# Optimization experiments

Hardware: AMD Instinct MI355X
Metric: run time of the kernel (lower is better)

The kernel has to match this reference:

```python
import jax, jax.numpy as jnp
import numpy as np

B, T, H, S, NH = 8, 4096, 1024, 64, 16
DH = H // NH
L = T // S  # tokens per sentence (contiguous partition)


def setup_inputs() -> dict:
    key = jax.random.key(0)
    ks = jax.random.split(key, 10)
    init = lambda k, shape: (jax.random.normal(k, shape, dtype=jnp.float32) * 0.02)
    starts = jnp.arange(S, dtype=jnp.int32) * L
    bounds = jnp.stack([starts, starts + L], axis=-1)  # [S,2]
    sentence_boundaries = jnp.broadcast_to(bounds, (B, S, 2))
    return {
        "context_hidden": jax.random.normal(ks[0], (B, T, H), dtype=jnp.float32),
        "sentence_boundaries": sentence_boundaries,
        "in_proj_w": init(ks[1], (3 * H, H)),
        "in_proj_b": jnp.zeros((3 * H,), jnp.float32),
        "out_w": init(ks[2], (H, H)),
        "out_b": jnp.zeros((H,), jnp.float32),
        "w1": init(ks[3], (H, 2 * H)),
        "b1": jnp.zeros((H,), jnp.float32),
        "w2": init(ks[4], (1, H)),
        "b2": jnp.zeros((1,), jnp.float32),
    }


def _forward(h, sentence_boundaries, in_proj_w, in_proj_b, out_w, out_b, w1, b1, w2, b2):
    starts = sentence_boundaries[:, :, 0]  # [B,S]
    ends = sentence_boundaries[:, :, 1]    # [B,S]
    t = jnp.arange(T, dtype=jnp.int32)
    # membership: token t belongs to sentence s iff start <= t < end
    member = (t[None, :, None] >= starts[:, None, :]) & (t[None, :, None] < ends[:, None, :])  # [B,T,S]
    mf = member.astype(h.dtype)
    counts = jnp.clip(mf.sum(axis=1), 1.0)  # [B,S]
    # segment mean pooling (encode_sentences)
    sent_repr = jnp.einsum('bts,bth->bsh', mf, h) / counts[..., None]  # [B,S,H]

    # multihead self-attention over sentence reprs (eval mode, no dropout)
    qkv = sent_repr @ in_proj_w.T + in_proj_b  # [B,S,3H]
    q, k, v = jnp.split(qkv, 3, axis=-1)
    q = q.reshape(B, S, NH, DH)
    k = k.reshape(B, S, NH, DH)
    v = v.reshape(B, S, NH, DH)
    scores = jnp.einsum('bqhd,bkhd->bhqk', q, k) / jnp.sqrt(jnp.asarray(DH, h.dtype))
    attn = jax.nn.softmax(scores, axis=-1)
    ctx = jnp.einsum('bhqk,bkhd->bqhd', attn, v).reshape(B, S, H)
    attended = ctx @ out_w.T + out_b  # [B,S,H]

    # gather each token's sentence repr
    sid = jnp.clip(member.astype(jnp.int32).argmax(axis=-1), 0, S - 1)  # [B,T]
    covered = member.any(axis=-1)  # [B,T]
    att_tok = jnp.take_along_axis(attended, sid[..., None], axis=1)  # [B,T,H]

    # coherence scorer MLP on concat([token, sent_repr]) without materializing concat
    hid = jax.nn.relu(h @ w1[:, :H].T + att_tok @ w1[:, H:].T + b1)  # [B,T,H]
    score = (hid @ w2.T + b2)[..., 0]  # [B,T]
    score = jnp.where(covered, score, 0.0)
    return h + score[..., None] * h


def reference(context_hidden, sentence_boundaries, in_proj_w, in_proj_b, out_w, out_b, w1, b1, w2, b2):
    return _forward(context_hidden, sentence_boundaries, in_proj_w, in_proj_b,
                    out_w, out_b, w1, b1, w2, b2)
```

## Files before the change

kernel.cpp:

```cpp
#include <hip/hip_runtime.h>
#include <stdint.h>

#define BB 8
#define TT 4096
#define HH 1024
#define SS 64
#define NHH 16
#define DHH 64

typedef __attribute__((ext_vector_type(8))) short short8;
typedef __attribute__((ext_vector_type(8))) unsigned short ushortx8;
typedef __attribute__((ext_vector_type(4))) float f32x4;
typedef unsigned short u16;

#define GLOAD16(gp, lp)                                                   \
  __builtin_amdgcn_global_load_lds(                                      \
      (const __attribute__((address_space(1))) void*)(gp),               \
      (__attribute__((address_space(3))) void*)(lp), 16, 0, 0)

__device__ __forceinline__ u16 f2bf(float f) {
  union { float f; uint32_t u; } v;
  v.f = f;
  uint32_t u = v.u;
  uint32_t r = u + 0x7fffu + ((u >> 16) & 1u);
  return (u16)(r >> 16);
}

__device__ __forceinline__ float bf2f(u16 b) {
  union { uint32_t u; float f; } v;
  v.u = ((uint32_t)b) << 16;
  return v.f;
}

__device__ __forceinline__ void stage_tile(u16* lds, const float* src, int ld, int tid) {
#pragma unroll
  for (int q = 0; q < 4; ++q) {
    int slot_id = tid + (q << 8);
    int row = slot_id >> 3;
    int sl = slot_id & 7;
    const float* p = src + (size_t)row * ld + (sl << 3);
    float4 x0 = *(const float4*)(p);
    float4 x1 = *(const float4*)(p + 4);
    ushortx8 o;
    o[0] = f2bf(x0.x); o[1] = f2bf(x0.y); o[2] = f2bf(x0.z); o[3] = f2bf(x0.w);
    o[4] = f2bf(x1.x); o[5] = f2bf(x1.y); o[6] = f2bf(x1.z); o[7] = f2bf(x1.w);
    *(ushortx8*)(&lds[(row << 6) + (((sl ^ (row & 7)) << 3))]) = o;
  }
}

__global__ __launch_bounds__(256) void conv_tile_kernel(const float* __restrict__ src,
                                                        int ld, int ntile_k,
                                                        u16* __restrict__ dst) {
  int bid = blockIdx.x;
  int rt = bid / ntile_k;
  int kt = bid - rt * ntile_k;
  const float* s0 = src + (size_t)rt * 128 * ld + kt * 64;
  u16* d0 = dst + (size_t)bid * 8192;
  int tid = threadIdx.x;
#pragma unroll
  for (int q = 0; q < 4; ++q) {
    int slot_id = tid + (q << 8);
    int row = slot_id >> 3;
    int sl = slot_id & 7;
    const float* p = s0 + (size_t)row * ld + (sl << 3);
    float4 x0 = *(const float4*)(p);
    float4 x1 = *(const float4*)(p + 4);
    ushortx8 o;
    o[0] = f2bf(x0.x); o[1] = f2bf(x0.y); o[2] = f2bf(x0.z); o[3] = f2bf(x0.w);
    o[4] = f2bf(x1.x); o[5] = f2bf(x1.y); o[6] = f2bf(x1.z); o[7] = f2bf(x1.w);
    *(ushortx8*)(&d0[(row << 6) + (((sl ^ (row & 7)) << 3))]) = o;
  }
}

__global__ __launch_bounds__(256) void pool_bf_kernel(const u16* __restrict__ hbf,
                                                      const int* __restrict__ bounds,
                                                      float* __restrict__ sent) {
  int bs = blockIdx.x;
  int b = bs >> 6;
  int start = bounds[bs * 2];
  int end = bounds[bs * 2 + 1];
  int lo = max(start, 0), hi = min(end, TT);
  int cnt = max(hi - lo, 0);
  float inv = 1.0f / (float)max(cnt, 1);
  int tid = threadIdx.x;
  int sg = tid >> 1;
  int half = tid & 1;
  int kt = sg >> 3, slot = sg & 7;
  float a[8] = {};
  for (int t = lo + half; t < hi; t += 2) {
    int grow = b * TT + t;
    int rt = grow >> 7, r = grow & 127;
    const u16* tile = hbf + ((size_t)rt * 16 + kt) * 8192;
    ushortx8 v = *(const ushortx8*)(&tile[(r << 6) + ((slot ^ (r & 7)) << 3)]);
#pragma unroll
    for (int j = 0; j < 8; ++j) a[j] += bf2f(v[j]);
  }
#pragma unroll
  for (int j = 0; j < 8; ++j) a[j] += __shfl_xor(a[j], 1);
  if (half == 0) {
    float* d = sent + (size_t)bs * HH + sg * 8;
#pragma unroll
    for (int j = 0; j < 8; ++j) d[j] = a[j] * inv;
  }
}

__global__ __launch_bounds__(256) void setup_misc(const float* __restrict__ ipb,
                                                  const float* __restrict__ outb,
                                                  const float* __restrict__ b1,
                                                  const int* __restrict__ bounds,
                                                  float* __restrict__ qkv,
                                                  float* __restrict__ att,
                                                  float* __restrict__ cbuf,
                                                  int* __restrict__ sid) {
  int idx = blockIdx.x * 256 + threadIdx.x;
  const int STR = 2048 * 256;
  for (int i = idx; i < 512 * 3072; i += STR) qkv[i] = ipb[i % 3072];
  for (int i = idx; i < 512 * 1024; i += STR) att[i] = outb[i & 1023];
  for (int i = idx; i < 512 * 1024; i += STR) cbuf[i] = b1[i & 1023];
  if (idx < BB * TT) {
    int b = idx >> 12, t = idx & (TT - 1);
    int r = -1;
    for (int s = 0; s < SS; ++s) {
      int st = bounds[(b * SS + s) * 2], en = bounds[(b * SS + s) * 2 + 1];
      if (t >= st && t < en) { r = s; break; }
    }
    sid[idx] = r;
  }
}

__global__ __launch_bounds__(256) void gemm_bt_atomic(const float* __restrict__ A, int lda,
                                                      const float* __restrict__ Bm, int ldb,
                                                      float* __restrict__ C, int ldc,
                                                      int kper) {
  __shared__ u16 As[128 * 64];
  __shared__ u16 Bs[128 * 64];
  int tid = threadIdx.x;
  int m0 = blockIdx.x * 128, n0 = blockIdx.y * 128;
  int kbeg = blockIdx.z * kper;
  f32x4 acc[4][4] = {};

  for (int k0 = kbeg; k0 < kbeg + kper; k0 += 64) {
    __syncthreads();
    stage_tile(As, A + (size_t)m0 * lda + k0, lda, tid);
    stage_tile(Bs, Bm + (size_t)n0 * ldb + k0, ldb, tid);
    __syncthreads();
    int lane = tid & 63, wid = tid >> 6;
    int wm = wid >> 1, wn = wid & 1;
    int lr = lane & 15, lg = lane >> 4;
#pragma unroll
    for (int kk = 0; kk < 2; ++kk) {
      short8 af[4], bfr[4];
#pragma unroll
      for (int i = 0; i < 4; ++i) {
        int arow = wm * 64 + i * 16 + lr;
        int aslot = (kk * 4 + lg) ^ (arow & 7);
        af[i] = *(const short8*)(&As[(arow << 6) + (aslot << 3)]);
        int brow = wn * 64 + i * 16 + lr;
        int bslot = (kk * 4 + lg) ^ (brow & 7);
        bfr[i] = *(const short8*)(&Bs[(brow << 6) + (bslot << 3)]);
      }
#pragma unroll
      for (int i = 0; i < 4; ++i)
#pragma unroll
        for (int j = 0; j < 4; ++j)
          acc[i][j] = __builtin_amdgcn_mfma_f32_16x16x32_bf16(af[i], bfr[j], acc[i][j], 0, 0, 0);
    }
  }

  int lane = tid & 63, wid = tid >> 6;
  int wm = wid >> 1, wn = wid & 1;
  int lr = lane & 15, lg = lane >> 4;
#pragma unroll
  for (int i = 0; i < 4; ++i)
#pragma unroll
    for (int j = 0; j < 4; ++j)
#pragma unroll
      for (int r = 0; r < 4; ++r) {
        int row = m0 + wm * 64 + i * 16 + lg * 4 + r;
        int col = n0 + wn * 64 + j * 16 + lr;
        atomicAdd(&C[(size_t)row * ldc + col], acc[i][j][r]);
      }
}

__global__ __launch_bounds__(256) void attn_kernel(const float* __restrict__ qkv,
                                                   float* __restrict__ ctx) {
  int bh = blockIdx.x;
  int b = bh >> 4, nh = bh & 15;
  __shared__ float q[64][64], k[64][64], v[64][64], s[64][64];
  int tid = threadIdx.x;
  const float* base = qkv + (size_t)b * SS * 3072 + nh * 64;
  for (int e = tid; e < 4096; e += 256) {
    int i = e >> 6, d = e & 63;
    q[i][d] = base[(size_t)i * 3072 + d];
    k[i][d] = base[(size_t)i * 3072 + 1024 + d];
    v[i][d] = base[(size_t)i * 3072 + 2048 + d];
  }
  __syncthreads();
  for (int e = tid; e < 4096; e += 256) {
    int i = e >> 6, j = e & 63;
    float acc = 0.f;
#pragma unroll 8
    for (int d = 0; d < 64; ++d) acc += q[i][d] * k[j][d];
    s[i][j] = acc * 0.125f;
  }
  __syncthreads();
  {
    int r = tid >> 2, sub = tid & 3;
    int j0 = sub * 16;
    float m = -1e30f;
#pragma unroll
    for (int j = 0; j < 16; ++j) m = fmaxf(m, s[r][j0 + j]);
    m = fmaxf(m, __shfl_xor(m, 1));
    m = fmaxf(m, __shfl_xor(m, 2));
    float sum = 0.f;
#pragma unroll
    for (int j = 0; j < 16; ++j) {
      float e_ = __expf(s[r][j0 + j] - m);
      s[r][j0 + j] = e_;
      sum += e_;
    }
    sum += __shfl_xor(sum, 1);
    sum += __shfl_xor(sum, 2);
    float inv = 1.0f / sum;
#pragma unroll
    for (int j = 0; j < 16; ++j) s[r][j0 + j] *= inv;
  }
  __syncthreads();
  for (int e = tid; e < 4096; e += 256) {
    int i = e >> 6, d = e & 63;
    float acc = 0.f;
#pragma unroll 8
    for (int j = 0; j < 64; ++j) acc += s[i][j] * v[j][d];
    ctx[((size_t)b * SS + i) * HH + nh * 64 + d] = acc;
  }
}

__global__ __launch_bounds__(512, 6) void score_partial(const u16* __restrict__ hbf,
                                                        const u16* __restrict__ wbf,
                                                        const float* __restrict__ cbuf,
                                                        const float* __restrict__ w2,
                                                        const int* __restrict__ sid_arr,
                                                        float* __restrict__ score_part) {
  __shared__ u16 As[8192];
  __shared__ u16 Bs[8192];
  __shared__ float w2_lds[128];
  __shared__ int sid_lds[128];
  __shared__ float red[128];

  int tid = threadIdx.x;
  int bid = blockIdx.x;
  int x = bid & 7;
  int g = bid >> 3;
  int mt = x * 32 + (g >> 3);
  int c = g & 7;
  int n0 = c * 128;
  size_t g0 = (size_t)mt * 128;
  int b = (int)(g0 >> 12);
  const u16* asrc = hbf + (size_t)mt * 16 * 8192;
  const u16* bsrc = wbf + (size_t)c * 16 * 8192;

  if (tid < 128) {
    w2_lds[tid] = w2[n0 + tid];
    sid_lds[tid] = sid_arr[g0 + tid];
    red[tid] = 0.f;
  }

  int lane = tid & 63, wid = tid >> 6;
  int wm = wid >> 2, wn = wid & 3;
  int lr = lane & 15, lg = lane >> 4;

  f32x4 acc[4][2] = {};
  for (int kt = 0; kt < 16; ++kt) {
    __syncthreads();
    const u16* at = asrc + kt * 8192;
    const u16* bt = bsrc + kt * 8192;
#pragma unroll
    for (int q = 0; q < 2; ++q) {
      int base = q * 4096 + wid * 512;
      GLOAD16(at + base + lane * 8, &As[base]);
      GLOAD16(bt + base + lane * 8, &Bs[base]);
    }
    __syncthreads();
#pragma unroll
    for (int kk = 0; kk < 2; ++kk) {
      short8 af[4], bfr[2];
#pragma unroll
      for (int i = 0; i < 4; ++i) {
        int arow = wm * 64 + i * 16 + lr;
        int aslot = (kk * 4 + lg) ^ (arow & 7);
        af[i] = *(const short8*)(&As[(arow << 6) + (aslot << 3)]);
      }
#pragma unroll
      for (int j = 0; j < 2; ++j) {
        int brow = wn * 32 + j * 16 + lr;
        int bslot = (kk * 4 + lg) ^ (brow & 7);
        bfr[j] = *(const short8*)(&Bs[(brow << 6) + (bslot << 3)]);
      }
#pragma unroll
      for (int i = 0; i < 4; ++i)
#pragma unroll
        for (int j = 0; j < 2; ++j)
          acc[i][j] = __builtin_amdgcn_mfma_f32_16x16x32_bf16(af[i], bfr[j], acc[i][j], 0, 0, 0);
    }
  }

  float sp[4][4];
#pragma unroll
  for (int i = 0; i < 4; ++i) {
#pragma unroll
    for (int r = 0; r < 4; ++r) {
      int rowl = wm * 64 + i * 16 + lg * 4 + r;
      int s = sid_lds[rowl];
      int sc = s < 0 ? 0 : s;
      const float* crow = cbuf + ((size_t)b * SS + sc) * HH + n0;
      float accs = 0.f;
#pragma unroll
      for (int j = 0; j < 2; ++j) {
        int coll = wn * 32 + j * 16 + lr;
        float t = acc[i][j][r] + crow[coll];
        if (t > 0.f) accs += t * w2_lds[coll];
      }
      sp[i][r] = accs;
    }
  }

#pragma unroll
  for (int i = 0; i < 4; ++i)
#pragma unroll
    for (int r = 0; r < 4; ++r) {
      float v = sp[i][r];
      v += __shfl_xor(v, 1);
      v += __shfl_xor(v, 2);
      v += __shfl_xor(v, 4);
      v += __shfl_xor(v, 8);
      sp[i][r] = v;
    }
  if (lr == 0) {
#pragma unroll
    for (int i = 0; i < 4; ++i)
#pragma unroll
      for (int r = 0; r < 4; ++r)
        atomicAdd(&red[wm * 64 + i * 16 + lg * 4 + r], sp[i][r]);
  }
  __syncthreads();
  if (tid < 128) score_part[(size_t)c * (BB * TT) + g0 + tid] = red[tid];
}

__global__ __launch_bounds__(256) void scale_kernel(const float* __restrict__ h,
                                                    const float* __restrict__ score_part,
                                                    const float* __restrict__ b2,
                                                    const int* __restrict__ sid_arr,
                                                    float* __restrict__ out) {
  __shared__ float fac[16];
  int tid = threadIdx.x;
  int r0 = blockIdx.x * 16;
  if (tid < 16) {
    int t = r0 + tid;
    float s = b2[0];
#pragma unroll
    for (int c = 0; c < 8; ++c) s += score_part[(size_t)c * (BB * TT) + t];
    fac[tid] = (sid_arr[t] >= 0) ? (1.0f + s) : 1.0f;
  }
  __syncthreads();
  const float4* h4 = (const float4*)h + (size_t)r0 * 256;
  float4* o4 = (float4*)out + (size_t)r0 * 256;
  for (int e = tid; e < 16 * 256; e += 256) {
    float f = fac[e >> 8];
    float4 v = h4[e];
    v.x *= f; v.y *= f; v.z *= f; v.w *= f;
    o4[e] = v;
  }
}

extern "C" void kernel_launch(void* const* d_in, const int* in_sizes, int n_in,
                              void* d_out, int out_size, void* d_ws, size_t ws_size,
                              hipStream_t stream) {
  const float* h        = (const float*)d_in[0];
  const int*   bounds   = (const int*)d_in[1];
  const float* in_proj_w = (const float*)d_in[2];
  const float* in_proj_b = (const float*)d_in[3];
  const float* out_w    = (const float*)d_in[4];
  const float* out_b    = (const float*)d_in[5];
  const float* w1       = (const float*)d_in[6];
  const float* b1       = (const float*)d_in[7];
  const float* w2       = (const float*)d_in[8];
  const float* b2       = (const float*)d_in[9];
  float* out = (float*)d_out;

  char* ws = (char*)d_ws;
  float* sent  = (float*)(ws);
  float* qkv   = (float*)(ws + (2ull << 20));
  float* ctx   = (float*)(ws + (8ull << 20));
  float* att   = (float*)(ws + (10ull << 20));
  float* cbuf  = (float*)(ws + (12ull << 20));
  int*   sid   = (int*)(ws + (14ull << 20));
  float* spart = (float*)(ws + (15ull << 20));
  u16*   hbf   = (u16*)(ws + (16ull << 20));
  u16*   wbf   = (u16*)(ws + (80ull << 20));

  conv_tile_kernel<<<256 * 16, 256, 0, stream>>>(h, HH, 16, hbf);
  conv_tile_kernel<<<8 * 16, 256, 0, stream>>>(w1, 2 * HH, 16, wbf);

  pool_bf_kernel<<<BB * SS, 256, 0, stream>>>(hbf, bounds, sent);
  setup_misc<<<2048, 256, 0, stream>>>(in_proj_b, out_b, b1, bounds, qkv, att, cbuf, sid);

  gemm_bt_atomic<<<dim3(4, 24, 4), 256, 0, stream>>>(sent, HH, in_proj_w, HH, qkv, 3 * HH, 256);
  attn_kernel<<<BB * NHH, 256, 0, stream>>>(qkv, ctx);
  gemm_bt_atomic<<<dim3(4, 8, 4), 256, 0, stream>>>(ctx, HH, out_w, HH, att, HH, 256);
  gemm_bt_atomic<<<dim3(4, 8, 4), 256, 0, stream>>>(att, HH, w1 + HH, 2 * HH, cbuf, HH, 256);

  score_partial<<<2048, 512, 0, stream>>>(hbf, wbf, cbuf, w2, sid, spart);
  scale_kernel<<<2048, 256, 0, stream>>>(h, spart, b2, sid, out);
}
```

Measured before the change: 300.4 us.

## Double-buffer score GEMM loads and fuse final scaling via last-block counter

The score GEMM now stages K-tiles into two LDS buffers two iterations ahead, using explicit vmcnt waits and barriers so global-to-LDS loads overlap MFMA work. The separate scale kernel is removed. Instead, the last of the eight column blocks for each row tile, found through an atomic counter, sums the partial scores and writes the scaled output. This saves a kernel launch and hides load latency. The cost is doubled LDS, lower occupancy (launch bound 6 down to 4), and a serialized tail in the finishing block.

```diff
diff --git a/kernel.cpp b/kernel.cpp
--- a/kernel.cpp
+++ b/kernel.cpp
@@ -17,6 +17,10 @@
   __builtin_amdgcn_global_load_lds(                                      \
       (const __attribute__((address_space(1))) void*)(gp),               \
       (__attribute__((address_space(3))) void*)(lp), 16, 0, 0)
+
+#define WAITVM(n)                                                         \
+  asm volatile("s_waitcnt vmcnt(" #n ")" ::: "memory");                  \
+  __builtin_amdgcn_sched_barrier(0)
 
 __device__ __forceinline__ u16 f2bf(float f) {
   union { float f; uint32_t u; } v;
@@ -111,12 +115,14 @@
                                                   float* __restrict__ qkv,
                                                   float* __restrict__ att,
                                                   float* __restrict__ cbuf,
-                                                  int* __restrict__ sid) {
+                                                  int* __restrict__ sid,
+                                                  int* __restrict__ cnt) {
   int idx = blockIdx.x * 256 + threadIdx.x;
   const int STR = 2048 * 256;
   for (int i = idx; i < 512 * 3072; i += STR) qkv[i] = ipb[i % 3072];
   for (int i = idx; i < 512 * 1024; i += STR) att[i] = outb[i & 1023];
   for (int i = idx; i < 512 * 1024; i += STR) cbuf[i] = b1[i & 1023];
+  if (idx < 256) cnt[idx] = 0;
   if (idx < BB * TT) {
     int b = idx >> 12, t = idx & (TT - 1);
     int r = -1;
@@ -235,17 +241,22 @@
   }
 }
 
-__global__ __launch_bounds__(512, 6) void score_partial(const u16* __restrict__ hbf,
+__global__ __launch_bounds__(512, 4) void score_partial(const u16* __restrict__ hbf,
                                                         const u16* __restrict__ wbf,
                                                         const float* __restrict__ cbuf,
                                                         const float* __restrict__ w2,
                                                         const int* __restrict__ sid_arr,
-                                                        float* __restrict__ score_part) {
-  __shared__ u16 As[8192];
-  __shared__ u16 Bs[8192];
+                                                        const float* __restrict__ h,
+                                                        const float* __restrict__ b2,
+                                                        float* __restrict__ score_part,
+                                                        int* __restrict__ cnt,
+                                                        float* __restrict__ out) {
+  __shared__ u16 Abuf[2][8192];
+  __shared__ u16 Bbuf[2][8192];
   __shared__ float w2_lds[128];
   __shared__ int sid_lds[128];
   __shared__ float red[128];
+  __shared__ int lastflag;
 
   int tid = threadIdx.x;
   int bid = blockIdx.x;
@@ -264,31 +275,43 @@
     sid_lds[tid] = sid_arr[g0 + tid];
     red[tid] = 0.f;
   }
+  asm volatile("s_waitcnt vmcnt(0)" ::: "memory");
+  __builtin_amdgcn_sched_barrier(0);
 
   int lane = tid & 63, wid = tid >> 6;
   int wm = wid >> 2, wn = wid & 3;
   int lr = lane & 15, lg = lane >> 4;
 
+#define STAGE_KT(kt, bufi)                                                \
+  {                                                                       \
+    const u16* at_ = asrc + (kt) * 8192;                                  \
+    const u16* bt_ = bsrc + (kt) * 8192;                                  \
+    _Pragma("unroll")                                                     \
+    for (int q = 0; q < 2; ++q) {                                         \
+      int base_ = q * 4096 + wid * 512;                                   \
+      GLOAD16(at_ + base_ + lane * 8, &Abuf[bufi][base_]);                \
+      GLOAD16(bt_ + base_ + lane * 8, &Bbuf[bufi][base_]);                \
+    }                                                                     \
+  }
+
+  STAGE_KT(0, 0);
+  STAGE_KT(1, 1);
+
   f32x4 acc[4][2] = {};
-  for (int kt = 0; kt < 16; ++kt) {
-    __syncthreads();
-    const u16* at = asrc + kt * 8192;
-    const u16* bt = bsrc + kt * 8192;
-#pragma unroll
-    for (int q = 0; q < 2; ++q) {
-      int base = q * 4096 + wid * 512;
-      GLOAD16(at + base + lane * 8, &As[base]);
-      GLOAD16(bt + base + lane * 8, &Bs[base]);
-    }
-    __syncthreads();
+  for (int i = 0; i < 16; ++i) {
+    if (i < 15) { WAITVM(4); } else { WAITVM(0); }
+    __builtin_amdgcn_s_barrier();
+    __builtin_amdgcn_sched_barrier(0);
+    const u16* As = Abuf[i & 1];
+    const u16* Bs = Bbuf[i & 1];
 #pragma unroll
     for (int kk = 0; kk < 2; ++kk) {
       short8 af[4], bfr[2];
 #pragma unroll
-      for (int i = 0; i < 4; ++i) {
-        int arow = wm * 64 + i * 16 + lr;
+      for (int ii = 0; ii < 4; ++ii) {
+        int arow = wm * 64 + ii * 16 + lr;
         int aslot = (kk * 4 + lg) ^ (arow & 7);
-        af[i] = *(const short8*)(&As[(arow << 6) + (aslot << 3)]);
+        af[ii] = *(const short8*)(&As[(arow << 6) + (aslot << 3)]);
       }
 #pragma unroll
       for (int j = 0; j < 2; ++j) {
@@ -297,12 +320,16 @@
         bfr[j] = *(const short8*)(&Bs[(brow << 6) + (bslot << 3)]);
       }
 #pragma unroll
-      for (int i = 0; i < 4; ++i)
+      for (int ii = 0; ii < 4; ++ii)
 #pragma unroll
         for (int j = 0; j < 2; ++j)
-          acc[i][j] = __builtin_amdgcn_mfma_f32_16x16x32_bf16(af[i], bfr[j], acc[i][j], 0, 0, 0);
-    }
-  }
+          acc[ii][j] = __builtin_amdgcn_mfma_f32_16x16x32_bf16(af[ii], bfr[j], acc[ii][j], 0, 0, 0);
+    }
+    __builtin_amdgcn_s_barrier();
+    __builtin_amdgcn_sched_barrier(0);
+    if (i < 14) STAGE_KT(i + 2, i & 1);
+  }
+#undef STAGE_KT
 
   float sp[4][4];
 #pragma unroll
@@ -344,31 +371,27 @@
   }
   __syncthreads();
   if (tid < 128) score_part[(size_t)c * (BB * TT) + g0 + tid] = red[tid];
-}
-
-__global__ __launch_bounds__(256) void scale_kernel(const float* __restrict__ h,
-                                                    const float* __restrict__ score_part,
-                                                    const float* __restrict__ b2,
-                                                    const int* __restrict__ sid_arr,
-                                                    float* __restrict__ out) {
-  __shared__ float fac[16];
-  int tid = threadIdx.x;
-  int r0 = blockIdx.x * 16;
-  if (tid < 16) {
-    int t = r0 + tid;
-    float s = b2[0];
-#pragma unroll
-    for (int c = 0; c < 8; ++c) s += score_part[(size_t)c * (BB * TT) + t];
-    fac[tid] = (sid_arr[t] >= 0) ? (1.0f + s) : 1.0f;
-  }
-  __syncthreads();
-  const float4* h4 = (const float4*)h + (size_t)r0 * 256;
-  float4* o4 = (float4*)out + (size_t)r0 * 256;
-  for (int e = tid; e < 16 * 256; e += 256) {
-    float f = fac[e >> 8];
-    float4 v = h4[e];
-    v.x *= f; v.y *= f; v.z *= f; v.w *= f;
-    o4[e] = v;
+  __threadfence();
+  __syncthreads();
+  if (tid == 0) lastflag = (atomicAdd(&cnt[mt], 1) == 7);
+  __syncthreads();
+  if (lastflag) {
+    __threadfence();
+    if (tid < 128) {
+      float s = b2[0];
+#pragma unroll
+      for (int cc = 0; cc < 8; ++cc) s += score_part[(size_t)cc * (BB * TT) + g0 + tid];
+      red[tid] = (sid_lds[tid] >= 0) ? (1.0f + s) : 1.0f;
+    }
+    __syncthreads();
+    const float4* h4 = (const float4*)h + g0 * 256;
+    float4* o4 = (float4*)out + g0 * 256;
+    for (int e = tid; e < 128 * 256; e += 512) {
+      float f = red[e >> 8];
+      float4 v = h4[e];
+      v.x *= f; v.y *= f; v.z *= f; v.w *= f;
+      o4[e] = v;
+    }
   }
 }
 
@@ -394,6 +417,7 @@
   float* att   = (float*)(ws + (10ull << 20));
   float* cbuf  = (float*)(ws + (12ull << 20));
   int*   sid   = (int*)(ws + (14ull << 20));
+  int*   cnt   = (int*)(ws + (14ull << 20) + (512 << 10));
   float* spart = (float*)(ws + (15ull << 20));
   u16*   hbf   = (u16*)(ws + (16ull << 20));
   u16*   wbf   = (u16*)(ws + (80ull << 20));
@@ -402,13 +426,12 @@
   conv_tile_kernel<<<8 * 16, 256, 0, stream>>>(w1, 2 * HH, 16, wbf);
 
   pool_bf_kernel<<<BB * SS, 256, 0, stream>>>(hbf, bounds, sent);
-  setup_misc<<<2048, 256, 0, stream>>>(in_proj_b, out_b, b1, bounds, qkv, att, cbuf, sid);
+  setup_misc<<<2048, 256, 0, stream>>>(in_proj_b, out_b, b1, bounds, qkv, att, cbuf, sid, cnt);
 
   gemm_bt_atomic<<<dim3(4, 24, 4), 256, 0, stream>>>(sent, HH, in_proj_w, HH, qkv, 3 * HH, 256);
   attn_kernel<<<BB * NHH, 256, 0, stream>>>(qkv, ctx);
   gemm_bt_atomic<<<dim3(4, 8, 4), 256, 0, stream>>>(ctx, HH, out_w, HH, att, HH, 256);
   gemm_bt_atomic<<<dim3(4, 8, 4), 256, 0, stream>>>(att, HH, w1 + HH, 2 * HH, cbuf, HH, 256);
 
-  score_partial<<<2048, 512, 0, stream>>>(hbf, wbf, cbuf, w2, sid, spart);
-  scale_kernel<<<2048, 256, 0, stream>>>(h, spart, b2, sid, out);
-}
+  score_partial<<<2048, 512, 0, stream>>>(hbf, wbf, cbuf, w2, sid, h, b2, spart, cnt, out);
+}
```

Result: slower. 875.3 us (+191.4%).
